# Optimization experiments

Hardware: AMD Instinct MI355X
Metric: run time of the kernel (lower is better)

Reference implementation:

```python
import jax, jax.numpy as jnp
import numpy as np
import math

B, N, D, K, H = 64, 16384, 64, 8, 128
ITERS = 3
LN_EPS = 1e-5  # torch LayerNorm default


def _ln(x, w, b):
    m = jnp.mean(x, axis=-1, keepdims=True)
    v = jnp.mean((x - m) ** 2, axis=-1, keepdims=True)
    return (x - m) * jax.lax.rsqrt(v + LN_EPS) * w + b


def setup_inputs() -> dict:
    key = jax.random.key(0)
    ks = jax.random.split(key, 20)
    s = 1.0 / math.sqrt(D)
    inp = {
        "inputs": jax.random.normal(ks[0], (B, N, D), jnp.float32),
        "noise": jax.random.normal(ks[1], (B, K, D), jnp.float32),
        "slots_mu": jax.random.normal(ks[2], (1, 1, D), jnp.float32),
        "slots_sigma": jax.random.uniform(ks[3], (1, 1, D), jnp.float32, -s, s),
        "ln_in_w": jnp.ones((D,), jnp.float32), "ln_in_b": jnp.zeros((D,), jnp.float32),
        "ln_slots_w": jnp.ones((D,), jnp.float32), "ln_slots_b": jnp.zeros((D,), jnp.float32),
        "ln_ff_w": jnp.ones((D,), jnp.float32), "ln_ff_b": jnp.zeros((D,), jnp.float32),
        "wk": jax.random.uniform(ks[4], (D, D), jnp.float32, -s, s),
        "bk": jax.random.uniform(ks[5], (D,), jnp.float32, -s, s),
        "wq": jax.random.uniform(ks[6], (D, D), jnp.float32, -s, s),
        "bq": jax.random.uniform(ks[7], (D,), jnp.float32, -s, s),
        "wv": jax.random.uniform(ks[8], (D, D), jnp.float32, -s, s),
        "bv": jax.random.uniform(ks[9], (D,), jnp.float32, -s, s),
        "gru_wih": jax.random.uniform(ks[10], (D, 3 * D), jnp.float32, -s, s),
        "gru_bih": jax.random.uniform(ks[11], (3 * D,), jnp.float32, -s, s),
        "gru_whh": jax.random.uniform(ks[12], (D, 3 * D), jnp.float32, -s, s),
        "gru_bhh": jax.random.uniform(ks[13], (3 * D,), jnp.float32, -s, s),
        "mlp_w1": jax.random.uniform(ks[14], (D, H), jnp.float32, -s, s),
        "mlp_b1": jax.random.uniform(ks[15], (H,), jnp.float32, -s, s),
        "mlp_w2": jax.random.uniform(ks[16], (H, D), jnp.float32, -1.0 / math.sqrt(H), 1.0 / math.sqrt(H)),
        "mlp_b2": jax.random.uniform(ks[17], (D,), jnp.float32, -1.0 / math.sqrt(H), 1.0 / math.sqrt(H)),
    }
    return inp


def reference(inputs, noise, slots_mu, slots_sigma, ln_in_w, ln_in_b,
              ln_slots_w, ln_slots_b, ln_ff_w, ln_ff_b,
              wk, bk, wq, bq, wv, bv,
              gru_wih, gru_bih, gru_whh, gru_bhh,
              mlp_w1, mlp_b1, mlp_w2, mlp_b2):
    x = _ln(inputs, ln_in_w, ln_in_b)              # [B, N, D]
    # k, v depend only on (fixed) inputs; original recomputes them each iter
    # with identical values, so hoist for efficiency (same math).
    k = x @ wk + bk                                 # [B, N, D]
    v = x @ wv + bv                                 # [B, N, D]
    slots = slots_mu + slots_sigma * noise          # [B, K, D]
    scale = 1.0 / math.sqrt(D)
    for _ in range(ITERS):
        prev = slots
        q = _ln(slots, ln_slots_w, ln_slots_b) @ wq + bq          # [B, K, D]
        logits = jnp.einsum('bkd,bnd->bkn', q, k) * scale          # [B, K, N]
        attn = jax.nn.softmax(logits, axis=1)  # softmax over slots
        updates = jnp.einsum('bkn,bnd->bkd', attn, v)              # [B, K, D]
        # torch GRUCell: gates ordered (r, z, n)
        gi = updates @ gru_wih + gru_bih                           # [B, K, 3D]
        gh = prev @ gru_whh + gru_bhh
        i_r, i_z, i_n = jnp.split(gi, 3, axis=-1)
        h_r, h_z, h_n = jnp.split(gh, 3, axis=-1)
        r = jax.nn.sigmoid(i_r + h_r)
        z = jax.nn.sigmoid(i_z + h_z)
        n = jnp.tanh(i_n + r * h_n)
        slots = (1.0 - z) * n + z * prev
        h = _ln(slots, ln_ff_w, ln_ff_b)
        slots = slots + (jax.nn.relu(h @ mlp_w1 + mlp_b1) @ mlp_w2 + mlp_b2)
    return slots
```

## Files before the change

### kernel.cpp

```cpp
#include <hip/hip_runtime.h>
#include <math.h>

#define B_ 64
#define N_ 16384
#define K_ 8
#define SCALE 0.125f
#define LN_EPS 1e-5f
#define CHUNKS 16
#define REC 528

typedef unsigned int u32;
typedef __fp16 half2_t __attribute__((ext_vector_type(2)));

__device__ __forceinline__ float wsum64(float v) {
#pragma unroll
  for (int m = 1; m < 64; m <<= 1) v += __shfl_xor(v, m);
  return v;
}

__device__ __forceinline__ u32 pk16(float a, float b) {
  half2_t h = __builtin_amdgcn_cvt_pkrtz(a, b);
  return __builtin_bit_cast(u32, h);
}
__device__ __forceinline__ float2 up16(u32 u) {
  half2_t h = __builtin_bit_cast(half2_t, u);
  return make_float2((float)h.x, (float)h.y);
}

__global__ void init_slots(const float* __restrict__ noise, const float* __restrict__ mu,
                           const float* __restrict__ sg, float* __restrict__ slots) {
  int i = blockIdx.x * blockDim.x + threadIdx.x;
  int d = i & 63;
  slots[i] = mu[d] + sg[d] * noise[i];
}

__global__ __launch_bounds__(64) void prep_q(
    const float* __restrict__ slots,
    const float* __restrict__ lnsw, const float* __restrict__ lnsb,
    const float* __restrict__ wq, const float* __restrict__ bq,
    const float* __restrict__ wk, const float* __restrict__ bk,
    const float* __restrict__ lniw, const float* __restrict__ lnib,
    float* __restrict__ qprep) {
  const int bk_i = blockIdx.x;
  const int b = bk_i >> 3, kk = bk_i & 7;
  const int d = threadIdx.x;
  __shared__ float xs[64], qsh[64], wkl[64 * 65];
  for (int i = 0; i < 64; ++i) wkl[i * 65 + d] = wk[i * 64 + d];
  float s = slots[bk_i * 64 + d];
  float m = wsum64(s) * (1.f / 64.f);
  float df = s - m;
  float var = wsum64(df * df) * (1.f / 64.f);
  float r = 1.f / sqrtf(var + LN_EPS);
  xs[d] = df * r * lnsw[d] + lnsb[d];
  __syncthreads();
  float q = bq[d];
  for (int c = 0; c < 64; ++c) q += xs[c] * wq[c * 64 + d];
  qsh[d] = q;
  __syncthreads();
  float qp = 0.f, c0 = 0.f;
  for (int dd = 0; dd < 64; ++dd) {
    float qd = qsh[dd];
    qp += wkl[d * 65 + dd] * qd;
    c0 += qd * bk[dd];
  }
  float qw = qp * lniw[d] * SCALE;
  float As = wsum64(qw);
  float Bp = wsum64(qp * lnib[d]);
  float Bc = (Bp + c0) * SCALE;
  float* rec = qprep + b * REC;
  rec[d * 8 + kk] = qw;
  if (d == 0) { rec[512 + kk] = As; rec[520 + kk] = Bc; }
}

__global__ __launch_bounds__(256, 4) void attn_pass(
    const float* __restrict__ inp, const float* __restrict__ qprep,
    float* __restrict__ part) {
  __shared__ u32 xls[4][64 * 34];
  __shared__ u32 awl[4][64 * 5];
  __shared__ float redST[64];
  const int tid = threadIdx.x;
  const int w = tid >> 6, lane = tid & 63;
  const int b = blockIdx.x >> 4, chunk = blockIdx.x & 15;
  const float* __restrict__ qp = qprep + b * REC;
  const float* srcw = inp + ((size_t)b * N_ + (size_t)(chunk * 1024 + w * 256)) * 64;
  float As_[8], Bc_[8];
#pragma unroll
  for (int kq = 0; kq < 8; ++kq) { As_[kq] = qp[512 + kq]; Bc_[kq] = qp[520 + kq]; }
  u32* __restrict__ xw = xls[w];
  u32* __restrict__ aww = awl[w];
  const int rh = lane >> 5, kh = (lane >> 3) & 3, c8 = lane & 7;
  float Y0[8] = {0, 0, 0, 0, 0, 0, 0, 0};
  float Y1[8] = {0, 0, 0, 0, 0, 0, 0, 0};
  float sS[8] = {0, 0, 0, 0, 0, 0, 0, 0};
  float sT[8] = {0, 0, 0, 0, 0, 0, 0, 0};
  for (int mt = 0; mt < 4; ++mt) {
    const float4* src = reinterpret_cast<const float4*>(srcw + (size_t)(mt * 64 + lane) * 64);
    float sum = 0.f, sq = 0.f;
    float l[8] = {0, 0, 0, 0, 0, 0, 0, 0};
#pragma unroll
    for (int j = 0; j < 16; ++j) {
      const float4 xv = src[j];
      const float xc[4] = {xv.x, xv.y, xv.z, xv.w};
#pragma unroll
      for (int e = 0; e < 4; ++e) {
        const int c = j * 4 + e;
        const float v = xc[e];
        sum += v; sq += v * v;
#pragma unroll
        for (int kq = 0; kq < 8; ++kq) l[kq] += qp[c * 8 + kq] * v;
      }
      *reinterpret_cast<uint2*>(&xw[lane * 34 + j * 2]) =
          make_uint2(pk16(xv.x, xv.y), pk16(xv.z, xv.w));
    }
    const float m = sum * (1.f / 64.f);
    const float var = sq * (1.f / 64.f) - m * m;
    const float r = 1.f / sqrtf(var + LN_EPS);
    const float mr = m * r;
    float lmax = -1e30f;
#pragma unroll
    for (int kq = 0; kq < 8; ++kq) {
      l[kq] = r * l[kq] - mr * As_[kq] + Bc_[kq];
      lmax = fmaxf(lmax, l[kq]);
    }
    float es = 0.f;
#pragma unroll
    for (int kq = 0; kq < 8; ++kq) { l[kq] = __expf(l[kq] - lmax); es += l[kq]; }
    const float inv = 1.f / es;
#pragma unroll
    for (int kq = 0; kq < 8; ++kq) {
      const float a = l[kq] * inv;
      sS[kq] += a;
      sT[kq] += a * mr;
      l[kq] = a * r;
    }
#pragma unroll
    for (int kh2 = 0; kh2 < 4; ++kh2)
      aww[lane * 5 + kh2] = pk16(l[2 * kh2], l[2 * kh2 + 1]);
#pragma unroll 4
    for (int i = 0; i < 32; ++i) {
      const int row = rh * 32 + i;
      const float2 ap = up16(aww[row * 5 + kh]);
      const uint2 q0 = *reinterpret_cast<const uint2*>(&xw[row * 34 + c8 * 4]);
      const uint2 q1 = *reinterpret_cast<const uint2*>(&xw[row * 34 + c8 * 4 + 2]);
      const u32 uu[4] = {q0.x, q0.y, q1.x, q1.y};
#pragma unroll
      for (int t = 0; t < 4; ++t) {
        const float2 xp = up16(uu[t]);
        Y0[2 * t]     += ap.x * xp.x;  Y0[2 * t + 1] += ap.x * xp.y;
        Y1[2 * t]     += ap.y * xp.x;  Y1[2 * t + 1] += ap.y * xp.y;
      }
    }
  }
#pragma unroll
  for (int kq = 0; kq < 8; ++kq) { sS[kq] = wsum64(sS[kq]); sT[kq] = wsum64(sT[kq]); }
  if (lane == 0) {
#pragma unroll
    for (int i = 0; i < 8; ++i) { redST[w * 16 + i] = sS[i]; redST[w * 16 + 8 + i] = sT[i]; }
  }
#pragma unroll
  for (int e = 0; e < 8; ++e) {
    Y0[e] += __shfl_xor(Y0[e], 32);
    Y1[e] += __shfl_xor(Y1[e], 32);
  }
  float* yr = reinterpret_cast<float*>(xw);
  if (lane < 32) {
#pragma unroll
    for (int e = 0; e < 8; ++e) {
      yr[(2 * kh + 0) * 64 + c8 * 8 + e] = Y0[e];
      yr[(2 * kh + 1) * 64 + c8 * 8 + e] = Y1[e];
    }
  }
  __syncthreads();
  float* dst = part + (size_t)blockIdx.x * REC;
  for (int o = tid; o < 512; o += 256) {
    float v = 0.f;
#pragma unroll
    for (int ww = 0; ww < 4; ++ww) v += reinterpret_cast<const float*>(xls[ww])[o];
    dst[o] = v;
  }
  if (tid < 16)
    dst[512 + tid] = redST[tid] + redST[16 + tid] + redST[32 + tid] + redST[48 + tid];
}

__global__ __launch_bounds__(256) void slot_update(
    const float* __restrict__ part, const float* slots_in,
    const float* __restrict__ lniw, const float* __restrict__ lnib,
    const float* __restrict__ wv, const float* __restrict__ bv,
    const float* __restrict__ wih, const float* __restrict__ bih,
    const float* __restrict__ whh, const float* __restrict__ bhh,
    const float* __restrict__ lnfw, const float* __restrict__ lnfb,
    const float* __restrict__ w1, const float* __restrict__ b1,
    const float* __restrict__ w2, const float* __restrict__ b2,
    const float* __restrict__ lnsw, const float* __restrict__ lnsb,
    const float* __restrict__ wq, const float* __restrict__ bq,
    const float* __restrict__ wk, const float* __restrict__ bkv,
    float* slots_out, float* __restrict__ qprep, const int do_prep) {
  const int bk_i = blockIdx.x, b = bk_i >> 3, kk = bk_i & 7;
  const int tid = threadIdx.x, cq = tid >> 6, d = tid & 63;
  const int c0 = cq * 16;
  __shared__ float pA[4][68], pB[4][68], pC[4][68], pD[4][68];
  __shared__ float xsh[64], psh[64], ush[64], hsh[64], snsh[64], qsh[64];
  __shared__ float hid1[2][132];
  const float* pb = part + (size_t)(b * CHUNKS) * REC;
  float S = 0.f, T1 = 0.f;
#pragma unroll
  for (int ch = 0; ch < CHUNKS; ++ch) {
    S += pb[ch * REC + 512 + kk];
    T1 += pb[ch * REC + 520 + kk];
  }
  {
    float y = 0.f;
#pragma unroll
    for (int cc = 0; cc < 4; ++cc)
      y += pb[(size_t)(cq * 4 + cc) * REC + kk * 64 + d];
    pA[cq][d] = y;
  }
  const float prev = slots_in[bk_i * 64 + d];
  if (cq == 0) psh[d] = prev;
  __syncthreads();
  if (cq == 0) {
    const float Y = pA[0][d] + pA[1][d] + pA[2][d] + pA[3][d];
    xsh[d] = lniw[d] * (Y - T1) + lnib[d] * S;
  }
  __syncthreads();
  {
    float up = 0.f, h0 = 0.f, h1 = 0.f, h2 = 0.f;
    for (int c = c0; c < c0 + 16; ++c) {
      const float xc = xsh[c], pc = psh[c];
      up += wv[c * 64 + d] * xc;
      h0 += pc * whh[c * 192 + d];
      h1 += pc * whh[c * 192 + 64 + d];
      h2 += pc * whh[c * 192 + 128 + d];
    }
    pA[cq][d] = up; pB[cq][d] = h0; pC[cq][d] = h1; pD[cq][d] = h2;
  }
  __syncthreads();
  float hh0 = 0.f, hh1 = 0.f, hh2 = 0.f;
  if (cq == 0) {
    ush[d] = S * bv[d] + pA[0][d] + pA[1][d] + pA[2][d] + pA[3][d];
    hh0 = bhh[d] + pB[0][d] + pB[1][d] + pB[2][d] + pB[3][d];
    hh1 = bhh[64 + d] + pC[0][d] + pC[1][d] + pC[2][d] + pC[3][d];
    hh2 = bhh[128 + d] + pD[0][d] + pD[1][d] + pD[2][d] + pD[3][d];
  }
  __syncthreads();
  {
    float g0 = 0.f, g1 = 0.f, g2 = 0.f;
    for (int c = c0; c < c0 + 16; ++c) {
      const float uc = ush[c];
      g0 += uc * wih[c * 192 + d];
      g1 += uc * wih[c * 192 + 64 + d];
      g2 += uc * wih[c * 192 + 128 + d];
    }
    pA[cq][d] = g0; pB[cq][d] = g1; pC[cq][d] = g2;
  }
  __syncthreads();
  if (cq == 0) {
    const float gi0 = bih[d] + pA[0][d] + pA[1][d] + pA[2][d] + pA[3][d];
    const float gi1 = bih[64 + d] + pB[0][d] + pB[1][d] + pB[2][d] + pB[3][d];
    const float gi2 = bih[128 + d] + pC[0][d] + pC[1][d] + pC[2][d] + pC[3][d];
    const float rg = 1.f / (1.f + __expf(-(gi0 + hh0)));
    const float zg = 1.f / (1.f + __expf(-(gi1 + hh1)));
    const float ng = tanhf(gi2 + rg * hh2);
    const float sn = (1.f - zg) * ng + zg * prev;
    const float mm = wsum64(sn) * (1.f / 64.f);
    const float df = sn - mm;
    const float vv = wsum64(df * df) * (1.f / 64.f);
    const float rr = 1.f / sqrtf(vv + LN_EPS);
    snsh[d] = sn;
    hsh[d] = df * rr * lnfw[d] + lnfb[d];
  }
  __syncthreads();
  {
    const int j = tid & 127, ch2 = tid >> 7;
    float a = 0.f;
    for (int c = ch2 * 32; c < ch2 * 32 + 32; ++c) a += hsh[c] * w1[c * 128 + j];
    hid1[ch2][j] = a;
  }
  __syncthreads();
  {
    float o = 0.f;
    for (int j2 = cq * 32; j2 < cq * 32 + 32; ++j2) {
      const float hv = fmaxf(hid1[0][j2] + hid1[1][j2] + b1[j2], 0.f);
      o += hv * w2[j2 * 64 + d];
    }
    pA[cq][d] = o;
  }
  __syncthreads();
  float news = 0.f;
  if (cq == 0) {
    news = snsh[d] + b2[d] + pA[0][d] + pA[1][d] + pA[2][d] + pA[3][d];
    slots_out[bk_i * 64 + d] = news;
  }
  if (!do_prep) return;
  if (cq == 0) {
    const float mm = wsum64(news) * (1.f / 64.f);
    const float df = news - mm;
    const float vv = wsum64(df * df) * (1.f / 64.f);
    const float rr = 1.f / sqrtf(vv + LN_EPS);
    xsh[d] = df * rr * lnsw[d] + lnsb[d];
  }
  __syncthreads();
  {
    float qpt = 0.f;
    for (int c = c0; c < c0 + 16; ++c) qpt += xsh[c] * wq[c * 64 + d];
    pB[cq][d] = qpt;
  }
  __syncthreads();
  if (cq == 0) qsh[d] = bq[d] + pB[0][d] + pB[1][d] + pB[2][d] + pB[3][d];
  __syncthreads();
  {
    float qq = 0.f;
    for (int dd2 = c0; dd2 < c0 + 16; ++dd2) qq += wk[d * 64 + dd2] * qsh[dd2];
    pC[cq][d] = qq;
  }
  __syncthreads();
  if (cq == 0) {
    const float qpv = pC[0][d] + pC[1][d] + pC[2][d] + pC[3][d];
    const float c0v = wsum64(qsh[d] * bkv[d]);
    const float qw = qpv * lniw[d] * SCALE;
    const float As = wsum64(qw);
    const float Bp = wsum64(qpv * lnib[d]);
    const float Bc = (Bp + c0v) * SCALE;
    float* rec = qprep + b * REC;
    rec[d * 8 + kk] = qw;
    if (d == 0) { rec[512 + kk] = As; rec[520 + kk] = Bc; }
  }
}

extern "C" void kernel_launch(void* const* d_in, const int* in_sizes, int n_in,
                              void* d_out, int out_size, void* d_ws, size_t ws_size,
                              hipStream_t stream) {
  const float* inp   = (const float*)d_in[0];
  const float* noise = (const float*)d_in[1];
  const float* mu    = (const float*)d_in[2];
  const float* sg    = (const float*)d_in[3];
  const float* lniw  = (const float*)d_in[4];
  const float* lnib  = (const float*)d_in[5];
  const float* lnsw  = (const float*)d_in[6];
  const float* lnsb  = (const float*)d_in[7];
  const float* lnfw  = (const float*)d_in[8];
  const float* lnfb  = (const float*)d_in[9];
  const float* wk    = (const float*)d_in[10];
  const float* bk    = (const float*)d_in[11];
  const float* wq    = (const float*)d_in[12];
  const float* bq    = (const float*)d_in[13];
  const float* wv    = (const float*)d_in[14];
  const float* bv    = (const float*)d_in[15];
  const float* wih   = (const float*)d_in[16];
  const float* bih   = (const float*)d_in[17];
  const float* whh   = (const float*)d_in[18];
  const float* bhh   = (const float*)d_in[19];
  const float* w1    = (const float*)d_in[20];
  const float* b1    = (const float*)d_in[21];
  const float* w2    = (const float*)d_in[22];
  const float* b2    = (const float*)d_in[23];
  float* ws = (float*)d_ws;
  float* slots = ws;
  float* qprep = ws + 32768;
  float* part  = ws + 32768 + 64 * REC;
  float* out   = (float*)d_out;
  init_slots<<<64, 512, 0, stream>>>(noise, mu, sg, slots);
  prep_q<<<B_ * K_, 64, 0, stream>>>(slots, lnsw, lnsb, wq, bq, wk, bk, lniw, lnib, qprep);
  for (int it = 0; it < 3; ++it) {
    attn_pass<<<B_ * CHUNKS, 256, 0, stream>>>(inp, qprep, part);
    slot_update<<<B_ * K_, 256, 0, stream>>>(
        part, slots, lniw, lnib, wv, bv, wih, bih, whh, bhh,
        lnfw, lnfb, w1, b1, w2, b2, lnsw, lnsb, wq, bq, wk, bk,
        (it == 2) ? out : slots, qprep, (it < 2) ? 1 : 0);
  }
}
```

Before: 319.3 us.

## Stage attention tiles in fp32 swizzled LDS with coalesced register prefetch

After: 663.2 us. 108% more time.

```diff
diff --git a/kernel.cpp b/kernel.cpp
--- a/kernel.cpp
+++ b/kernel.cpp
@@ -9,22 +9,10 @@
 #define CHUNKS 16
 #define REC 528
 
-typedef unsigned int u32;
-typedef __fp16 half2_t __attribute__((ext_vector_type(2)));
-
 __device__ __forceinline__ float wsum64(float v) {
 #pragma unroll
   for (int m = 1; m < 64; m <<= 1) v += __shfl_xor(v, m);
   return v;
-}
-
-__device__ __forceinline__ u32 pk16(float a, float b) {
-  half2_t h = __builtin_amdgcn_cvt_pkrtz(a, b);
-  return __builtin_bit_cast(u32, h);
-}
-__device__ __forceinline__ float2 up16(u32 u) {
-  half2_t h = __builtin_bit_cast(half2_t, u);
-  return make_float2((float)h.x, (float)h.y);
 }
 
 __global__ void init_slots(const float* __restrict__ noise, const float* __restrict__ mu,
@@ -72,11 +60,11 @@
   if (d == 0) { rec[512 + kk] = As; rec[520 + kk] = Bc; }
 }
 
-__global__ __launch_bounds__(256, 4) void attn_pass(
+__global__ __launch_bounds__(256, 2) void attn_pass(
     const float* __restrict__ inp, const float* __restrict__ qprep,
     float* __restrict__ part) {
-  __shared__ u32 xls[4][64 * 34];
-  __shared__ u32 awl[4][64 * 5];
+  __shared__ __align__(16) float xls[4][64 * 64];
+  __shared__ __align__(16) float awl[4][64 * 12];
   __shared__ float redST[64];
   const int tid = threadIdx.x;
   const int w = tid >> 6, lane = tid & 63;
@@ -86,40 +74,59 @@
   float As_[8], Bc_[8];
 #pragma unroll
   for (int kq = 0; kq < 8; ++kq) { As_[kq] = qp[512 + kq]; Bc_[kq] = qp[520 + kq]; }
-  u32* __restrict__ xw = xls[w];
-  u32* __restrict__ aww = awl[w];
-  const int rh = lane >> 5, kh = (lane >> 3) & 3, c8 = lane & 7;
-  float Y0[8] = {0, 0, 0, 0, 0, 0, 0, 0};
-  float Y1[8] = {0, 0, 0, 0, 0, 0, 0, 0};
-  float sS[8] = {0, 0, 0, 0, 0, 0, 0, 0};
-  float sT[8] = {0, 0, 0, 0, 0, 0, 0, 0};
+  float* __restrict__ xw = xls[w];
+  float* __restrict__ aww = awl[w];
+  const int g = lane >> 4, c = lane & 15;
+  const int cl = c & 7, ch = c & 8;
+  float Y[8][4];
+  float sS[8], sT[8];
+#pragma unroll
+  for (int kq = 0; kq < 8; ++kq) {
+    sS[kq] = 0.f; sT[kq] = 0.f;
+#pragma unroll
+    for (int e = 0; e < 4; ++e) Y[kq][e] = 0.f;
+  }
+  float4 xr[16];
+#pragma unroll
+  for (int i = 0; i < 16; ++i)
+    xr[i] = *reinterpret_cast<const float4*>(srcw + (size_t)(4 * i + g) * 64 + c * 4);
   for (int mt = 0; mt < 4; ++mt) {
-    const float4* src = reinterpret_cast<const float4*>(srcw + (size_t)(mt * 64 + lane) * 64);
+#pragma unroll
+    for (int i = 0; i < 16; ++i) {
+      const int row = 4 * i + g;
+      const int phys = ch | (cl ^ (row & 7));
+      *reinterpret_cast<float4*>(&xw[row * 64 + phys * 4]) = xr[i];
+    }
+    if (mt < 3) {
+#pragma unroll
+      for (int i = 0; i < 16; ++i)
+        xr[i] = *reinterpret_cast<const float4*>(
+            srcw + (size_t)((mt + 1) * 64 + 4 * i + g) * 64 + c * 4);
+    }
     float sum = 0.f, sq = 0.f;
     float l[8] = {0, 0, 0, 0, 0, 0, 0, 0};
 #pragma unroll
     for (int j = 0; j < 16; ++j) {
-      const float4 xv = src[j];
+      const int phys = (j & 8) | ((j & 7) ^ (lane & 7));
+      const float4 xv = *reinterpret_cast<const float4*>(&xw[lane * 64 + phys * 4]);
       const float xc[4] = {xv.x, xv.y, xv.z, xv.w};
 #pragma unroll
       for (int e = 0; e < 4; ++e) {
-        const int c = j * 4 + e;
+        const int cc = j * 4 + e;
         const float v = xc[e];
         sum += v; sq += v * v;
 #pragma unroll
-        for (int kq = 0; kq < 8; ++kq) l[kq] += qp[c * 8 + kq] * v;
+        for (int kq = 0; kq < 8; ++kq) l[kq] += qp[cc * 8 + kq] * v;
       }
-      *reinterpret_cast<uint2*>(&xw[lane * 34 + j * 2]) =
-          make_uint2(pk16(xv.x, xv.y), pk16(xv.z, xv.w));
     }
     const float m = sum * (1.f / 64.f);
     const float var = sq * (1.f / 64.f) - m * m;
-    const float r = 1.f / sqrtf(var + LN_EPS);
-    const float mr = m * r;
+    const float rs = 1.f / sqrtf(var + LN_EPS);
+    const float mr = m * rs;
     float lmax = -1e30f;
 #pragma unroll
     for (int kq = 0; kq < 8; ++kq) {
-      l[kq] = r * l[kq] - mr * As_[kq] + Bc_[kq];
+      l[kq] = rs * l[kq] - mr * As_[kq] + Bc_[kq];
       lmax = fmaxf(lmax, l[kq]);
     }
     float es = 0.f;
@@ -131,24 +138,23 @@
       const float a = l[kq] * inv;
       sS[kq] += a;
       sT[kq] += a * mr;
-      l[kq] = a * r;
-    }
-#pragma unroll
-    for (int kh2 = 0; kh2 < 4; ++kh2)
-      aww[lane * 5 + kh2] = pk16(l[2 * kh2], l[2 * kh2 + 1]);
-#pragma unroll 4
-    for (int i = 0; i < 32; ++i) {
-      const int row = rh * 32 + i;
-      const float2 ap = up16(aww[row * 5 + kh]);
-      const uint2 q0 = *reinterpret_cast<const uint2*>(&xw[row * 34 + c8 * 4]);
-      const uint2 q1 = *reinterpret_cast<const uint2*>(&xw[row * 34 + c8 * 4 + 2]);
-      const u32 uu[4] = {q0.x, q0.y, q1.x, q1.y};
-#pragma unroll
-      for (int t = 0; t < 4; ++t) {
-        const float2 xp = up16(uu[t]);
-        Y0[2 * t]     += ap.x * xp.x;  Y0[2 * t + 1] += ap.x * xp.y;
-        Y1[2 * t]     += ap.y * xp.x;  Y1[2 * t + 1] += ap.y * xp.y;
-      }
+      l[kq] = a * rs;
+    }
+    *reinterpret_cast<float4*>(&aww[lane * 12])     = make_float4(l[0], l[1], l[2], l[3]);
+    *reinterpret_cast<float4*>(&aww[lane * 12 + 4]) = make_float4(l[4], l[5], l[6], l[7]);
+#pragma unroll
+    for (int t = 0; t < 16; ++t) {
+      const int row = 4 * t + g;
+      const float4 a0 = *reinterpret_cast<const float4*>(&aww[row * 12]);
+      const float4 a1 = *reinterpret_cast<const float4*>(&aww[row * 12 + 4]);
+      const int phys = ch | (cl ^ (row & 7));
+      const float4 xv = *reinterpret_cast<const float4*>(&xw[row * 64 + phys * 4]);
+      const float xc[4] = {xv.x, xv.y, xv.z, xv.w};
+      const float aa[8] = {a0.x, a0.y, a0.z, a0.w, a1.x, a1.y, a1.z, a1.w};
+#pragma unroll
+      for (int kq = 0; kq < 8; ++kq)
+#pragma unroll
+        for (int e = 0; e < 4; ++e) Y[kq][e] += aa[kq] * xc[e];
     }
   }
 #pragma unroll
@@ -158,26 +164,22 @@
     for (int i = 0; i < 8; ++i) { redST[w * 16 + i] = sS[i]; redST[w * 16 + 8 + i] = sT[i]; }
   }
 #pragma unroll
-  for (int e = 0; e < 8; ++e) {
-    Y0[e] += __shfl_xor(Y0[e], 32);
-    Y1[e] += __shfl_xor(Y1[e], 32);
-  }
-  float* yr = reinterpret_cast<float*>(xw);
-  if (lane < 32) {
-#pragma unroll
-    for (int e = 0; e < 8; ++e) {
-      yr[(2 * kh + 0) * 64 + c8 * 8 + e] = Y0[e];
-      yr[(2 * kh + 1) * 64 + c8 * 8 + e] = Y1[e];
-    }
+  for (int kq = 0; kq < 8; ++kq)
+#pragma unroll
+    for (int e = 0; e < 4; ++e) {
+      Y[kq][e] += __shfl_xor(Y[kq][e], 16);
+      Y[kq][e] += __shfl_xor(Y[kq][e], 32);
+    }
+  if (lane < 16) {
+#pragma unroll
+    for (int kq = 0; kq < 8; ++kq)
+      *reinterpret_cast<float4*>(&aww[kq * 64 + lane * 4]) =
+          make_float4(Y[kq][0], Y[kq][1], Y[kq][2], Y[kq][3]);
   }
   __syncthreads();
   float* dst = part + (size_t)blockIdx.x * REC;
-  for (int o = tid; o < 512; o += 256) {
-    float v = 0.f;
-#pragma unroll
-    for (int ww = 0; ww < 4; ++ww) v += reinterpret_cast<const float*>(xls[ww])[o];
-    dst[o] = v;
-  }
+  for (int o = tid; o < 512; o += 256)
+    dst[o] = awl[0][o] + awl[1][o] + awl[2][o] + awl[3][o];
   if (tid < 16)
     dst[512 + tid] = redST[tid] + redST[16 + tid] + redST[32 + tid] + redST[48 + tid];
 }
```
